# Kernel optimization log

Hardware: AMD Instinct MI355X
Metric: run time of the kernel (lower is better)

Reference implementation:

```python
import jax, jax.numpy as jnp
import numpy as np

H = 1024      # hidden_size
VIN = 32000   # input_size (source vocab)
VOUT = 32000  # output_size (target vocab)
S = 256       # src length
T = 256       # trg length


def setup_inputs() -> dict:
    key = jax.random.key(0)
    ks = jax.random.split(key, 16)
    def n(k, shape):
        return jax.random.normal(k, shape, dtype=jnp.float32) * 0.02
    return {
        "src": jax.random.randint(ks[0], (S,), 0, VIN, dtype=jnp.int32),
        "trg": jax.random.randint(ks[1], (T,), 0, VOUT, dtype=jnp.int32),
        "start": jnp.zeros((1,), dtype=jnp.int32),
        "enc_emb": n(ks[2], (VIN, H)),
        "enc_Wih": n(ks[3], (4 * H, H)),
        "enc_Whh": n(ks[4], (4 * H, H)),
        "enc_bih": n(ks[5], (4 * H,)),
        "enc_bhh": n(ks[6], (4 * H,)),
        "dec_emb": n(ks[7], (VOUT, H)),
        "dec_Wih": n(ks[8], (4 * H, H)),
        "dec_Whh": n(ks[9], (4 * H, H)),
        "dec_bih": n(ks[10], (4 * H,)),
        "dec_bhh": n(ks[11], (4 * H,)),
        "lin_W": n(ks[12], (VOUT, H)),
        "lin_b": n(ks[13], (VOUT,)),
    }


def _lstm_cell(x, h, c, Wih, Whh, bih, bhh):
    # PyTorch gate order: input, forget, cell(g), output
    gates = x @ Wih.T + bih + h @ Whh.T + bhh  # [4H]
    i, f, g, o = jnp.split(gates, 4)
    i = jax.nn.sigmoid(i)
    f = jax.nn.sigmoid(f)
    g = jnp.tanh(g)
    o = jax.nn.sigmoid(o)
    c = f * c + i * g
    h = o * jnp.tanh(c)
    return h, c


def reference(src, trg, start, enc_emb, enc_Wih, enc_Whh, enc_bih, enc_bhh,
              dec_emb, dec_Wih, dec_Whh, dec_bih, dec_bhh, lin_W, lin_b):
    hdim = enc_Wih.shape[1]
    h0 = jnp.zeros((hdim,), dtype=enc_emb.dtype)

    # --- encoder: scan over src tokens (batch=1, unbatched state) ---
    enc_x = enc_emb[src]  # [S, H]
    def estep(carry, x):
        h, c = carry
        h, c = _lstm_cell(x, h, c, enc_Wih, enc_Whh, enc_bih, enc_bhh)
        return (h, c), None
    (h, c), _ = jax.lax.scan(estep, (h0, h0), enc_x)

    # --- decoder: teacher forcing ratio 1 -> input is start, trg[:-1] ---
    dec_in = jnp.concatenate([start, trg[:-1]])  # [T]
    dec_x = dec_emb[dec_in]  # [T, H]
    def dstep(carry, x):
        h, c = carry
        h, c = _lstm_cell(x, h, c, dec_Wih, dec_Whh, dec_bih, dec_bhh)
        logits = h @ lin_W.T + lin_b  # [VOUT]  (dropout p=0 is identity)
        return (h, c), jax.nn.log_softmax(logits)
    _, pred = jax.lax.scan(dstep, (h, c), dec_x)
    return pred  # [T, VOUT]
```

## Files before the change

kernel.cpp:

```cpp
#include <hip/hip_runtime.h>
#include <hip/hip_bf16.h>


#define HDIM 1024
#define SLEN 256
#define TLEN 256
#define VOUTN 32000
#define G4 4096
#define NWGC 128
#define HPW 8

typedef __bf16 bf16_t;
typedef __bf16 bf16x8 __attribute__((ext_vector_type(8)));
typedef float f32x4 __attribute__((ext_vector_type(4)));
typedef unsigned long long u64;

static __device__ inline bf16x8 cvt8(float4 a, float4 b) {
    bf16x8 r;
    r[0] = (__bf16)a.x; r[1] = (__bf16)a.y; r[2] = (__bf16)a.z; r[3] = (__bf16)a.w;
    r[4] = (__bf16)b.x; r[5] = (__bf16)b.y; r[6] = (__bf16)b.z; r[7] = (__bf16)b.w;
    return r;
}

static __device__ inline float sig_f(float x) {
    return 1.f / (1.f + __expf(-x));
}
static __device__ inline float tanh_f(float x) {
    float e = __expf(-2.f * fabsf(x));
    float r = (1.f - e) / (1.f + e);
    return copysignf(r, x);
}

__global__ __launch_bounds__(64) void xw_all(
    const int* __restrict__ src, const int* __restrict__ trg,
    const int* __restrict__ start,
    const float* __restrict__ enc_emb, const float* __restrict__ enc_Wih,
    const float* __restrict__ enc_bih, const float* __restrict__ enc_bhh,
    const float* __restrict__ dec_emb, const float* __restrict__ dec_Wih,
    const float* __restrict__ dec_bih, const float* __restrict__ dec_bhh,
    float* __restrict__ encXW, float* __restrict__ decXW,
    u64* __restrict__ hseq)
{
    const int b = blockIdx.x, tid = threadIdx.x;

    for (size_t i = (size_t)b * 64 + tid; i < (size_t)512 * 1024; i += (size_t)512 * 64)
        hseq[i] = 0ULL;

    const bool enc = (b < 256);
    const int*   toks = enc ? src : trg;
    const float* emb  = enc ? enc_emb : dec_emb;
    const float* W    = enc ? enc_Wih : dec_Wih;
    const float* bi   = enc ? enc_bih : dec_bih;
    const float* bh   = enc ? enc_bhh : dec_bhh;
    float*       outp = enc ? encXW : decXW;

    __shared__ int stok[SLEN];
    for (int i = tid; i < SLEN; i += 64)
        stok[i] = enc ? toks[i] : (i == 0 ? start[0] : toks[i - 1]);
    __syncthreads();

    const int l15 = tid & 15, quad = tid >> 4;
    const int n = (b & 255) * 16 + l15;
    const float* wrow = W + (size_t)n * HDIM + quad * 8;

    f32x4 acc[16] = {};
    for (int kt = 0; kt < HDIM / 32; ++kt) {
        float4 b0 = *(const float4*)(wrow + kt * 32);
        float4 b1 = *(const float4*)(wrow + kt * 32 + 4);
        bf16x8 bf = cvt8(b0, b1);
#pragma unroll
        for (int mt = 0; mt < 16; ++mt) {
            const float* ar = emb + (size_t)stok[mt * 16 + l15] * HDIM + kt * 32 + quad * 8;
            bf16x8 af = cvt8(*(const float4*)ar, *(const float4*)(ar + 4));
            acc[mt] = __builtin_amdgcn_mfma_f32_16x16x32_bf16(af, bf, acc[mt], 0, 0, 0);
        }
    }
    float bias = bi[n] + bh[n];
#pragma unroll
    for (int mt = 0; mt < 16; ++mt)
#pragma unroll
        for (int r = 0; r < 4; ++r) {
            int t = mt * 16 + quad * 4 + r;
            outp[(size_t)t * G4 + n] = acc[mt][r] + bias;
        }
}

__global__ __launch_bounds__(256, 1) void lstm_seq(
    const float* __restrict__ encXW,
    const float* __restrict__ decXW,
    const float* __restrict__ encWhh,
    const float* __restrict__ decWhh,
    u64* __restrict__ hseq,
    bf16_t* __restrict__ Hs)
{
    __shared__ float sh[HDIM + HDIM / 32];
    __shared__ float sg[32];

    const int tid = threadIdx.x;
    const int wg = blockIdx.x;
    const int wave = tid >> 6, lane = tid & 63;
    const int rg = (wave << 1) | (lane >> 5);
    const int ks = lane & 31;
    const int j0 = wg * HPW;

    float4 w[4][8];
    auto load_w = [&](const float* __restrict__ Wsrc) {
#pragma unroll
        for (int r = 0; r < 4; ++r) {
            int lr = rg * 4 + r;
            const float* srcp = Wsrc + (size_t)((lr >> 3) * HDIM + j0 + (lr & 7)) * HDIM + ks * 32;
#pragma unroll
            for (int i = 0; i < 8; ++i) w[r][i] = *(const float4*)(srcp + i * 4);
        }
    };
    load_w(encWhh);

    float creg = 0.f;

    for (int t = 0; t < SLEN + TLEN; ++t) {
        if (t == SLEN) load_w(decWhh);

        if (wave == 0) {
            if (t == 0) {
#pragma unroll
                for (int i = 0; i < 8; ++i) {
                    int j = lane * 8 + i;        sh[j + (j >> 5)] = 0.f;
                    int j2 = 512 + lane * 8 + i; sh[j2 + (j2 >> 5)] = 0.f;
                }
            } else {
                const u64* row = hseq + (size_t)t * HDIM;
                const unsigned tag = (unsigned)t;
                const u64* pa = row + lane * 8;
                const u64* pb = row + 512 + lane * 8;
                for (;;) {
                    u64 a0 = __hip_atomic_load(pa, __ATOMIC_RELAXED, __HIP_MEMORY_SCOPE_AGENT);
                    u64 b0 = __hip_atomic_load(pb, __ATOMIC_RELAXED, __HIP_MEMORY_SCOPE_AGENT);
                    if (__all(((unsigned)(a0 >> 32) == tag) && ((unsigned)(b0 >> 32) == tag)))
                        break;
                }
                u64 av[8], bv[8];
                for (;;) {
#pragma unroll
                    for (int i = 0; i < 8; ++i)
                        av[i] = __hip_atomic_load(pa + i, __ATOMIC_RELAXED, __HIP_MEMORY_SCOPE_AGENT);
#pragma unroll
                    for (int i = 0; i < 8; ++i)
                        bv[i] = __hip_atomic_load(pb + i, __ATOMIC_RELAXED, __HIP_MEMORY_SCOPE_AGENT);
                    bool ok = true;
#pragma unroll
                    for (int i = 0; i < 8; ++i)
                        ok = ok && ((unsigned)(av[i] >> 32) == tag)
                                && ((unsigned)(bv[i] >> 32) == tag);
                    if (__all(ok)) break;
                    __builtin_amdgcn_s_sleep(1);
                }
#pragma unroll
                for (int i = 0; i < 8; ++i) {
                    int j = lane * 8 + i;
                    sh[j + (j >> 5)] = __uint_as_float((unsigned)av[i]);
                    int j2 = 512 + lane * 8 + i;
                    sh[j2 + (j2 >> 5)] = __uint_as_float((unsigned)bv[i]);
                }
            }
        }
        __syncthreads();

        float xg0 = 0.f, xg1 = 0.f, xg2 = 0.f, xg3 = 0.f;
        if (tid < HPW) {
            const float* xw = (t < SLEN) ? encXW + (size_t)t * G4
                                         : decXW + (size_t)(t - SLEN) * G4;
            int j = j0 + tid;
            xg0 = xw[0 * HDIM + j];
            xg1 = xw[1 * HDIM + j];
            xg2 = xw[2 * HDIM + j];
            xg3 = xw[3 * HDIM + j];
        }

        float hv[32];
#pragma unroll
        for (int i = 0; i < 32; ++i) hv[i] = sh[ks * 33 + i];

        float s0 = 0.f, s1 = 0.f, s2 = 0.f, s3 = 0.f;
#pragma unroll
        for (int i = 0; i < 8; ++i) {
            float hx = hv[4 * i], hy = hv[4 * i + 1], hz = hv[4 * i + 2], hw = hv[4 * i + 3];
            s0 += w[0][i].x * hx + w[0][i].y * hy + w[0][i].z * hz + w[0][i].w * hw;
            s1 += w[1][i].x * hx + w[1][i].y * hy + w[1][i].z * hz + w[1][i].w * hw;
            s2 += w[2][i].x * hx + w[2][i].y * hy + w[2][i].z * hz + w[2][i].w * hw;
            s3 += w[3][i].x * hx + w[3][i].y * hy + w[3][i].z * hz + w[3][i].w * hw;
        }
        float ss[4] = {s0, s1, s2, s3};
#pragma unroll
        for (int r = 0; r < 4; ++r) {
            float s = ss[r];
            s += __shfl_down(s, 16, 32);
            s += __shfl_down(s, 8, 32);
            s += __shfl_down(s, 4, 32);
            s += __shfl_down(s, 2, 32);
            s += __shfl_down(s, 1, 32);
            if (ks == 0) sg[rg * 4 + r] = s;
        }
        __syncthreads();

        if (tid < HPW) {
            int j = j0 + tid;
            float gi = sg[0 * 8 + tid] + xg0;
            float gf = sg[1 * 8 + tid] + xg1;
            float gg = sg[2 * 8 + tid] + xg2;
            float go = sg[3 * 8 + tid] + xg3;
            float ii = sig_f(gi);
            float ff = sig_f(gf);
            float g  = tanh_f(gg);
            float oo = sig_f(go);
            float cn = ff * creg + ii * g;
            float hn = oo * tanh_f(cn);
            creg = cn;
            if (t >= SLEN) Hs[(size_t)(t - SLEN) * HDIM + j] = (bf16_t)hn;
            if (t < SLEN + TLEN - 1) {
                u64 pk = ((u64)(unsigned)(t + 1) << 32) | (u64)__float_as_uint(hn);
                __hip_atomic_store(hseq + (size_t)(t + 1) * HDIM + j, pk,
                                   __ATOMIC_RELAXED, __HIP_MEMORY_SCOPE_AGENT);
            }
        }
    }
}

__global__ __launch_bounds__(256) void out_gemm(
    const bf16_t* __restrict__ Hs,
    const float* __restrict__ W,
    const float* __restrict__ bias,
    float* __restrict__ out)
{
    int tid = threadIdx.x;
    int wave = tid >> 6, lane = tid & 63;
    int l15 = lane & 15, quad = lane >> 4;
    int n = (blockIdx.x * 4 + wave) * 16 + l15;
    const float* wrow = W + (size_t)n * HDIM + quad * 8;

    f32x4 acc[16] = {};
    for (int kt = 0; kt < HDIM / 32; ++kt) {
        float4 b0 = *(const float4*)(wrow + kt * 32);
        float4 b1 = *(const float4*)(wrow + kt * 32 + 4);
        bf16x8 bf = cvt8(b0, b1);
#pragma unroll
        for (int mt = 0; mt < 16; ++mt) {
            bf16x8 af = *(const bf16x8*)(Hs + (size_t)(mt * 16 + l15) * HDIM + kt * 32 + quad * 8);
            acc[mt] = __builtin_amdgcn_mfma_f32_16x16x32_bf16(af, bf, acc[mt], 0, 0, 0);
        }
    }
    float bv = bias[n];
#pragma unroll
    for (int mt = 0; mt < 16; ++mt)
#pragma unroll
        for (int r = 0; r < 4; ++r) {
            int t = mt * 16 + quad * 4 + r;
            out[(size_t)t * VOUTN + n] = acc[mt][r] + bv;
        }
}

__global__ __launch_bounds__(1024) void log_softmax_k(float* __restrict__ out)
{
    float* row = out + (size_t)blockIdx.x * VOUTN;
    float4* r4 = (float4*)row;
    const int tid = threadIdx.x;
    const int wave = tid >> 6, lane = tid & 63;
    __shared__ float sred[16];

    float m = -1e30f;
    for (int i = tid; i < VOUTN / 4; i += 1024) {
        float4 v = r4[i];
        m = fmaxf(fmaxf(fmaxf(m, v.x), fmaxf(v.y, v.z)), v.w);
    }
    for (int o = 32; o; o >>= 1) m = fmaxf(m, __shfl_down(m, o, 64));
    if (lane == 0) sred[wave] = m;
    __syncthreads();
    float bm = sred[0];
#pragma unroll
    for (int i = 1; i < 16; ++i) bm = fmaxf(bm, sred[i]);
    __syncthreads();

    float s = 0.f;
    for (int i = tid; i < VOUTN / 4; i += 1024) {
        float4 v = r4[i];
        s += __expf(v.x - bm) + __expf(v.y - bm) + __expf(v.z - bm) + __expf(v.w - bm);
    }
    for (int o = 32; o; o >>= 1) s += __shfl_down(s, o, 64);
    if (lane == 0) sred[wave] = s;
    __syncthreads();
    float S = 0.f;
#pragma unroll
    for (int i = 0; i < 16; ++i) S += sred[i];
    float lse = bm + __logf(S);

    for (int i = tid; i < VOUTN / 4; i += 1024) {
        float4 v = r4[i];
        v.x -= lse; v.y -= lse; v.z -= lse; v.w -= lse;
        r4[i] = v;
    }
}

extern "C" void kernel_launch(void* const* d_in, const int* in_sizes, int n_in,
                              void* d_out, int out_size, void* d_ws, size_t ws_size,
                              hipStream_t stream) {
    const int*   src     = (const int*)d_in[0];
    const int*   trg     = (const int*)d_in[1];
    const int*   start   = (const int*)d_in[2];
    const float* enc_emb = (const float*)d_in[3];
    const float* enc_Wih = (const float*)d_in[4];
    const float* enc_Whh = (const float*)d_in[5];
    const float* enc_bih = (const float*)d_in[6];
    const float* enc_bhh = (const float*)d_in[7];
    const float* dec_emb = (const float*)d_in[8];
    const float* dec_Wih = (const float*)d_in[9];
    const float* dec_Whh = (const float*)d_in[10];
    const float* dec_bih = (const float*)d_in[11];
    const float* dec_bhh = (const float*)d_in[12];
    const float* lin_W   = (const float*)d_in[13];
    const float* lin_b   = (const float*)d_in[14];
    float* out = (float*)d_out;

    char* ws = (char*)d_ws;
    float*  encXW = (float*)(ws);
    float*  decXW = (float*)(ws + 4194304);
    bf16_t* Hs    = (bf16_t*)(ws + 8388608);
    u64*    hseq  = (u64*)(ws + 9437184);

    xw_all<<<512, 64, 0, stream>>>(src, trg, start,
                                   enc_emb, enc_Wih, enc_bih, enc_bhh,
                                   dec_emb, dec_Wih, dec_bih, dec_bhh,
                                   encXW, decXW, hseq);

    lstm_seq<<<NWGC, 256, 0, stream>>>(encXW, decXW, enc_Whh, dec_Whh, hseq, Hs);

    out_gemm<<<500, 256, 0, stream>>>(Hs, lin_W, lin_b, out);
    log_softmax_k<<<256, 1024, 0, stream>>>(out);
}
```

Baseline: 2.297 ms.

## Spread hidden-state polling across all threads and keep each gate row in one half-wave

Each 32-lane group now owns one hidden unit and computes all four gate dot products for it. The gate sums are finished with a shuffle reduction and the cell update runs in registers, so the shared gate buffer and one mid-step barrier go away. Polling of the previous step's hidden state is spread over all 256 threads, each spinning on four entries, instead of wave 0 loading everything. A trailing barrier is added before the shared buffer is overwritten. The cost is more threads issuing atomic polls against global memory, and the cell update now runs on 8 lanes in separate waves.

```diff
diff --git a/kernel.cpp b/kernel.cpp
--- a/kernel.cpp
+++ b/kernel.cpp
@@ -94,23 +94,22 @@
     bf16_t* __restrict__ Hs)
 {
     __shared__ float sh[HDIM + HDIM / 32];
-    __shared__ float sg[32];
 
     const int tid = threadIdx.x;
     const int wg = blockIdx.x;
-    const int wave = tid >> 6, lane = tid & 63;
-    const int rg = (wave << 1) | (lane >> 5);
-    const int ks = lane & 31;
+    const int jl = tid >> 5;
+    const int ks = tid & 31;
     const int j0 = wg * HPW;
+    const bool fin = (ks == 0);
+    const int jfin = j0 + jl;
 
     float4 w[4][8];
     auto load_w = [&](const float* __restrict__ Wsrc) {
 #pragma unroll
-        for (int r = 0; r < 4; ++r) {
-            int lr = rg * 4 + r;
-            const float* srcp = Wsrc + (size_t)((lr >> 3) * HDIM + j0 + (lr & 7)) * HDIM + ks * 32;
-#pragma unroll
-            for (int i = 0; i < 8; ++i) w[r][i] = *(const float4*)(srcp + i * 4);
+        for (int g = 0; g < 4; ++g) {
+            const float* srcp = Wsrc + (size_t)(g * HDIM + j0 + jl) * HDIM + ks * 32;
+#pragma unroll
+            for (int i = 0; i < 8; ++i) w[g][i] = *(const float4*)(srcp + i * 4);
         }
     };
     load_w(encWhh);
@@ -120,61 +119,42 @@
     for (int t = 0; t < SLEN + TLEN; ++t) {
         if (t == SLEN) load_w(decWhh);
 
-        if (wave == 0) {
-            if (t == 0) {
-#pragma unroll
-                for (int i = 0; i < 8; ++i) {
-                    int j = lane * 8 + i;        sh[j + (j >> 5)] = 0.f;
-                    int j2 = 512 + lane * 8 + i; sh[j2 + (j2 >> 5)] = 0.f;
-                }
-            } else {
-                const u64* row = hseq + (size_t)t * HDIM;
-                const unsigned tag = (unsigned)t;
-                const u64* pa = row + lane * 8;
-                const u64* pb = row + 512 + lane * 8;
-                for (;;) {
-                    u64 a0 = __hip_atomic_load(pa, __ATOMIC_RELAXED, __HIP_MEMORY_SCOPE_AGENT);
-                    u64 b0 = __hip_atomic_load(pb, __ATOMIC_RELAXED, __HIP_MEMORY_SCOPE_AGENT);
-                    if (__all(((unsigned)(a0 >> 32) == tag) && ((unsigned)(b0 >> 32) == tag)))
-                        break;
-                }
-                u64 av[8], bv[8];
-                for (;;) {
-#pragma unroll
-                    for (int i = 0; i < 8; ++i)
-                        av[i] = __hip_atomic_load(pa + i, __ATOMIC_RELAXED, __HIP_MEMORY_SCOPE_AGENT);
-#pragma unroll
-                    for (int i = 0; i < 8; ++i)
-                        bv[i] = __hip_atomic_load(pb + i, __ATOMIC_RELAXED, __HIP_MEMORY_SCOPE_AGENT);
-                    bool ok = true;
-#pragma unroll
-                    for (int i = 0; i < 8; ++i)
-                        ok = ok && ((unsigned)(av[i] >> 32) == tag)
-                                && ((unsigned)(bv[i] >> 32) == tag);
-                    if (__all(ok)) break;
-                    __builtin_amdgcn_s_sleep(1);
-                }
-#pragma unroll
-                for (int i = 0; i < 8; ++i) {
-                    int j = lane * 8 + i;
-                    sh[j + (j >> 5)] = __uint_as_float((unsigned)av[i]);
-                    int j2 = 512 + lane * 8 + i;
-                    sh[j2 + (j2 >> 5)] = __uint_as_float((unsigned)bv[i]);
-                }
-            }
-        }
-        __syncthreads();
-
         float xg0 = 0.f, xg1 = 0.f, xg2 = 0.f, xg3 = 0.f;
-        if (tid < HPW) {
+        if (fin) {
             const float* xw = (t < SLEN) ? encXW + (size_t)t * G4
                                          : decXW + (size_t)(t - SLEN) * G4;
-            int j = j0 + tid;
-            xg0 = xw[0 * HDIM + j];
-            xg1 = xw[1 * HDIM + j];
-            xg2 = xw[2 * HDIM + j];
-            xg3 = xw[3 * HDIM + j];
-        }
+            xg0 = xw[0 * HDIM + jfin];
+            xg1 = xw[1 * HDIM + jfin];
+            xg2 = xw[2 * HDIM + jfin];
+            xg3 = xw[3 * HDIM + jfin];
+        }
+
+        const int q = tid << 2;
+        const int pad = q >> 5;
+        if (t == 0) {
+            sh[q + pad]     = 0.f;
+            sh[q + pad + 1] = 0.f;
+            sh[q + pad + 2] = 0.f;
+            sh[q + pad + 3] = 0.f;
+        } else {
+            const u64* hin = hseq + (size_t)t * HDIM + q;
+            const unsigned tag = (unsigned)t;
+            u64 v0, v1, v2, v3;
+            for (;;) {
+                v0 = __hip_atomic_load(hin + 0, __ATOMIC_RELAXED, __HIP_MEMORY_SCOPE_AGENT);
+                v1 = __hip_atomic_load(hin + 1, __ATOMIC_RELAXED, __HIP_MEMORY_SCOPE_AGENT);
+                v2 = __hip_atomic_load(hin + 2, __ATOMIC_RELAXED, __HIP_MEMORY_SCOPE_AGENT);
+                v3 = __hip_atomic_load(hin + 3, __ATOMIC_RELAXED, __HIP_MEMORY_SCOPE_AGENT);
+                if ((unsigned)(v0 >> 32) == tag && (unsigned)(v1 >> 32) == tag &&
+                    (unsigned)(v2 >> 32) == tag && (unsigned)(v3 >> 32) == tag) break;
+                __builtin_amdgcn_s_sleep(1);
+            }
+            sh[q + pad]     = __uint_as_float((unsigned)v0);
+            sh[q + pad + 1] = __uint_as_float((unsigned)v1);
+            sh[q + pad + 2] = __uint_as_float((unsigned)v2);
+            sh[q + pad + 3] = __uint_as_float((unsigned)v3);
+        }
+        __syncthreads();
 
         float hv[32];
 #pragma unroll
@@ -189,25 +169,19 @@
             s2 += w[2][i].x * hx + w[2][i].y * hy + w[2][i].z * hz + w[2][i].w * hw;
             s3 += w[3][i].x * hx + w[3][i].y * hy + w[3][i].z * hz + w[3][i].w * hw;
         }
-        float ss[4] = {s0, s1, s2, s3};
-#pragma unroll
-        for (int r = 0; r < 4; ++r) {
-            float s = ss[r];
-            s += __shfl_down(s, 16, 32);
-            s += __shfl_down(s, 8, 32);
-            s += __shfl_down(s, 4, 32);
-            s += __shfl_down(s, 2, 32);
-            s += __shfl_down(s, 1, 32);
-            if (ks == 0) sg[rg * 4 + r] = s;
-        }
-        __syncthreads();
-
-        if (tid < HPW) {
-            int j = j0 + tid;
-            float gi = sg[0 * 8 + tid] + xg0;
-            float gf = sg[1 * 8 + tid] + xg1;
-            float gg = sg[2 * 8 + tid] + xg2;
-            float go = sg[3 * 8 + tid] + xg3;
+#pragma unroll
+        for (int o = 16; o; o >>= 1) {
+            s0 += __shfl_down(s0, o, 32);
+            s1 += __shfl_down(s1, o, 32);
+            s2 += __shfl_down(s2, o, 32);
+            s3 += __shfl_down(s3, o, 32);
+        }
+
+        if (fin) {
+            float gi = s0 + xg0;
+            float gf = s1 + xg1;
+            float gg = s2 + xg2;
+            float go = s3 + xg3;
             float ii = sig_f(gi);
             float ff = sig_f(gf);
             float g  = tanh_f(gg);
@@ -215,13 +189,14 @@
             float cn = ff * creg + ii * g;
             float hn = oo * tanh_f(cn);
             creg = cn;
-            if (t >= SLEN) Hs[(size_t)(t - SLEN) * HDIM + j] = (bf16_t)hn;
+            if (t >= SLEN) Hs[(size_t)(t - SLEN) * HDIM + jfin] = (bf16_t)hn;
             if (t < SLEN + TLEN - 1) {
                 u64 pk = ((u64)(unsigned)(t + 1) << 32) | (u64)__float_as_uint(hn);
-                __hip_atomic_store(hseq + (size_t)(t + 1) * HDIM + j, pk,
+                __hip_atomic_store(hseq + (size_t)(t + 1) * HDIM + jfin, pk,
                                    __ATOMIC_RELAXED, __HIP_MEMORY_SCOPE_AGENT);
             }
         }
+        __syncthreads();
     }
 }
 
```

Measured after the change: 2.334 ms. No clear change (+1.6%).
